# Kernel optimization log

Hardware: AMD Instinct MI355X
Metric: run time of the kernel (lower is better)

The kernel has to match this reference:

```python
import jax, jax.numpy as jnp
import numpy as np

N_HEAD = 16
N_FEAT = 1024
D_K = N_FEAT // N_HEAD  # 64
BLOCK_SIZE = 32
MAX_BLOCKS = 512
CHUNK = 1024
OFFSET = 3072  # cache_seqlens[0]: frames already committed to the cache
SCALE = 0.02


def setup_inputs() -> dict:
    key = jax.random.key(0)
    ks = jax.random.split(key, 12)
    # logical -> physical block mapping: a fixed permutation (irregular access)
    rng = np.random.default_rng(0)
    block_table = jnp.asarray(rng.permutation(MAX_BLOCKS).astype(np.int32))[None, :]
    return {
        "x": jax.random.normal(ks[0], (1, CHUNK, N_FEAT), jnp.float32),
        "Wq": jax.random.normal(ks[1], (N_FEAT, N_FEAT), jnp.float32) * SCALE,
        "bq": jax.random.normal(ks[2], (N_FEAT,), jnp.float32) * SCALE,
        "Wk": jax.random.normal(ks[3], (N_FEAT, N_FEAT), jnp.float32) * SCALE,
        "bk": jax.random.normal(ks[4], (N_FEAT,), jnp.float32) * SCALE,
        "Wv": jax.random.normal(ks[5], (N_FEAT, N_FEAT), jnp.float32) * SCALE,
        "bv": jax.random.normal(ks[6], (N_FEAT,), jnp.float32) * SCALE,
        "Wo": jax.random.normal(ks[7], (N_FEAT, N_FEAT), jnp.float32) * SCALE,
        "bo": jax.random.normal(ks[8], (N_FEAT,), jnp.float32) * SCALE,
        "k_cache": jax.random.normal(ks[9], (MAX_BLOCKS, BLOCK_SIZE, N_HEAD, D_K), jnp.float32),
        "v_cache": jax.random.normal(ks[10], (MAX_BLOCKS, BLOCK_SIZE, N_HEAD, D_K), jnp.float32),
        "block_table": block_table,
        "seqlen_offset": OFFSET,
    }


def reference(x, Wq, bq, Wk, bk, Wv, bv, Wo, bo, k_cache, v_cache, block_table, seqlen_offset):
    B, T, _ = x.shape  # B == 1 (streaming decode)
    # forward_qkv: Q/K/V projections, split into heads
    q = (x @ Wq + bq).reshape(B, T, N_HEAD, D_K).transpose(0, 2, 1, 3)  # (1,h,T,d)
    k_new = (x @ Wk + bk).reshape(B, T, N_HEAD, D_K)                    # (1,T,h,d)
    v_new = (x @ Wv + bv).reshape(B, T, N_HEAD, D_K)

    # _paged_write_kv: scatter the chunk frames into the physical block pool
    pos = seqlen_offset + jnp.arange(T)              # absolute frame indices
    phys = block_table[0, pos // BLOCK_SIZE]         # physical block per frame
    off = pos % BLOCK_SIZE                           # offset within block
    k_cache = k_cache.at[phys, off].set(k_new[0])
    v_cache = v_cache.at[phys, off].set(v_new[0])

    # _paged_gather_kv: gather all total_frames (old + just-written) frames
    total = seqlen_offset + T
    nblk = (total + BLOCK_SIZE - 1) // BLOCK_SIZE
    bids = block_table[0, :nblk]
    kf = k_cache[bids].reshape(-1, N_HEAD, D_K)[:total]  # (total, h, d)
    vf = v_cache[bids].reshape(-1, N_HEAD, D_K)[:total]

    # SDPA over the gathered K/V (no mask; softmax in fp32 as in the source)
    scores = jnp.einsum('bhqd,khd->bhqk', q, kf) / np.float32(np.sqrt(D_K))
    attn = jax.nn.softmax(scores.astype(jnp.float32), axis=-1).astype(x.dtype)
    ctx = jnp.einsum('bhqk,khd->bhqd', attn, vf)         # (1,h,T,d)

    # forward_attention tail: merge heads + output projection
    out = ctx.transpose(0, 2, 1, 3).reshape(B, T, N_HEAD * D_K) @ Wo + bo
    return out
```

## Files before the change

### kernel.cpp

```cpp
#include <hip/hip_runtime.h>
#include <hip/hip_bf16.h>

#define NFEAT 1024
#define NHEAD 16
#define DK 64
#define TCHUNK 1024
#define MAXTOK 4096
#define NSPLIT 4

using bf16x8 = __attribute__((ext_vector_type(8))) short;
using f32x4  = __attribute__((ext_vector_type(4))) float;

__device__ __forceinline__ short f2bf(float f) {
    __hip_bfloat16 h = __float2bfloat16(f);
    return *reinterpret_cast<short*>(&h);
}

__device__ __forceinline__ float exp2fast(float x) {
    return __builtin_amdgcn_exp2f(x);
}

#define QSCALE 0.1803368801f

__global__ __launch_bounds__(256) void pack_kernel(
    const float* __restrict__ x,
    const float* __restrict__ Wq, const float* __restrict__ Wk,
    const float* __restrict__ Wv, const float* __restrict__ Wo,
    const float* __restrict__ kc, const float* __restrict__ vc,
    const int* __restrict__ btab, const int* __restrict__ soff,
    short* __restrict__ xb, short* __restrict__ Wt,
    short* __restrict__ kg, short* __restrict__ vt) {
    const int b = blockIdx.x;
    const int t = threadIdx.x;
    if (b < 1024) {
        __shared__ short T[64][72];
        const int w = b >> 8, tile = b & 255;
        const int k0 = (tile >> 4) << 6, n0 = (tile & 15) << 6;
        const float* W = (w == 0) ? Wq : (w == 1) ? Wk : (w == 2) ? Wv : Wo;
        const int r = t >> 2, cs = (t & 3) << 4;
        #pragma unroll
        for (int u = 0; u < 4; ++u) {
            float4 v = *reinterpret_cast<const float4*>(
                &W[(size_t)(k0 + r) * NFEAT + n0 + cs + u * 4]);
            T[cs + u * 4 + 0][r] = f2bf(v.x);
            T[cs + u * 4 + 1][r] = f2bf(v.y);
            T[cs + u * 4 + 2][r] = f2bf(v.z);
            T[cs + u * 4 + 3][r] = f2bf(v.w);
        }
        __syncthreads();
        const int c = t >> 2, rs = (t & 3) << 4;
        bf16x8 a0 = *reinterpret_cast<const bf16x8*>(&T[c][rs]);
        bf16x8 a1 = *reinterpret_cast<const bf16x8*>(&T[c][rs + 8]);
        size_t drow = (size_t)(w * 1024 + n0 + c) * NFEAT + k0 + rs;
        *reinterpret_cast<bf16x8*>(&Wt[drow]) = a0;
        *reinterpret_cast<bf16x8*>(&Wt[drow + 8]) = a1;
    } else if (b < 1152) {
        const int e0 = ((b - 1024) * 256 + t) * 32;
        #pragma unroll
        for (int u = 0; u < 4; ++u) {
            float4 v0 = *reinterpret_cast<const float4*>(&x[e0 + u * 8]);
            float4 v1 = *reinterpret_cast<const float4*>(&x[e0 + u * 8 + 4]);
            bf16x8 o;
            o[0] = f2bf(v0.x); o[1] = f2bf(v0.y); o[2] = f2bf(v0.z); o[3] = f2bf(v0.w);
            o[4] = f2bf(v1.x); o[5] = f2bf(v1.y); o[6] = f2bf(v1.z); o[7] = f2bf(v1.w);
            *reinterpret_cast<bf16x8*>(&xb[e0 + u * 8]) = o;
        }
    } else {
        __shared__ short TV[64][72];
        const int cb = b - 1152;
        const int h = cb & 15;
        const int t0 = (cb >> 4) << 6;
        const int offset = soff[0];
        const int row = t >> 2, ds = (t & 3) << 4;
        const int tok = t0 + row;
        short kv[16], vv[16];
        if (tok < offset) {
            int phys = btab[tok >> 5];
            size_t base = ((size_t)(phys * 32 + (tok & 31)) * NHEAD + h) * DK + ds;
            #pragma unroll
            for (int u = 0; u < 4; ++u) {
                float4 kf = *reinterpret_cast<const float4*>(&kc[base + u * 4]);
                float4 vf = *reinterpret_cast<const float4*>(&vc[base + u * 4]);
                kv[u * 4 + 0] = f2bf(kf.x); kv[u * 4 + 1] = f2bf(kf.y);
                kv[u * 4 + 2] = f2bf(kf.z); kv[u * 4 + 3] = f2bf(kf.w);
                vv[u * 4 + 0] = f2bf(vf.x); vv[u * 4 + 1] = f2bf(vf.y);
                vv[u * 4 + 2] = f2bf(vf.z); vv[u * 4 + 3] = f2bf(vf.w);
            }
        } else {
            #pragma unroll
            for (int e = 0; e < 16; ++e) { kv[e] = 0; vv[e] = 0; }
        }
        {
            bf16x8 a, bb;
            #pragma unroll
            for (int e = 0; e < 8; ++e) { a[e] = kv[e]; bb[e] = kv[8 + e]; }
            size_t kb = ((size_t)h * MAXTOK + tok) * DK + ds;
            *reinterpret_cast<bf16x8*>(&kg[kb]) = a;
            *reinterpret_cast<bf16x8*>(&kg[kb + 8]) = bb;
        }
        #pragma unroll
        for (int e = 0; e < 16; ++e) TV[ds + e][row] = vv[e];
        __syncthreads();
        {
            const int d = t >> 2, ts = (t & 3) << 4;
            bf16x8 a = *reinterpret_cast<const bf16x8*>(&TV[d][ts]);
            bf16x8 bb = *reinterpret_cast<const bf16x8*>(&TV[d][ts + 8]);
            size_t vb = ((size_t)h * DK + d) * MAXTOK + t0 + ts;
            *reinterpret_cast<bf16x8*>(&vt[vb]) = a;
            *reinterpret_cast<bf16x8*>(&vt[vb + 8]) = bb;
        }
    }
}

__global__ __launch_bounds__(256) void qkv_gemm(
    const short* __restrict__ xb, const short* __restrict__ Wt,
    const float* __restrict__ bq, const float* __restrict__ bk,
    const float* __restrict__ bv, const int* __restrict__ soff,
    short* __restrict__ qbuf, short* __restrict__ kg, short* __restrict__ vt) {
    __shared__ short As[64][72];
    __shared__ short Bs[128][72];
    const int tid = threadIdx.x;
    const int lane = tid & 63;
    const int w = tid >> 6;
    const int l15 = lane & 15, lg = lane >> 4;
    const int wr = w >> 1, wc = w & 1;
    const int m0 = blockIdx.y << 6, n0 = blockIdx.x << 7;
    const int sel = n0 >> 10;
    const float* bias = (sel == 0) ? bq : (sel == 1) ? bk : bv;

    f32x4 acc[2][4];
    #pragma unroll
    for (int i = 0; i < 2; ++i)
        #pragma unroll
        for (int j = 0; j < 4; ++j) acc[i][j] = (f32x4){0.f, 0.f, 0.f, 0.f};

    for (int k0 = 0; k0 < NFEAT; k0 += 64) {
        #pragma unroll
        for (int r = 0; r < 2; ++r) {
            int f = tid + (r << 8);
            int row = f >> 3, kc = (f & 7) << 3;
            *reinterpret_cast<bf16x8*>(&As[row][kc]) =
                *reinterpret_cast<const bf16x8*>(&xb[(size_t)(m0 + row) * NFEAT + k0 + kc]);
        }
        #pragma unroll
        for (int r = 0; r < 4; ++r) {
            int f = tid + (r << 8);
            int row = f >> 3, kc = (f & 7) << 3;
            *reinterpret_cast<bf16x8*>(&Bs[row][kc]) =
                *reinterpret_cast<const bf16x8*>(&Wt[(size_t)(n0 + row) * NFEAT + k0 + kc]);
        }
        __syncthreads();
        #pragma unroll
        for (int kk = 0; kk < 2; ++kk) {
            bf16x8 am[2], bn[4];
            #pragma unroll
            for (int mi = 0; mi < 2; ++mi)
                am[mi] = *reinterpret_cast<const bf16x8*>(
                    &As[wr * 32 + mi * 16 + l15][kk * 32 + lg * 8]);
            #pragma unroll
            for (int ni = 0; ni < 4; ++ni)
                bn[ni] = *reinterpret_cast<const bf16x8*>(
                    &Bs[wc * 64 + ni * 16 + l15][kk * 32 + lg * 8]);
            #pragma unroll
            for (int mi = 0; mi < 2; ++mi)
                #pragma unroll
                for (int ni = 0; ni < 4; ++ni)
                    acc[mi][ni] = __builtin_amdgcn_mfma_f32_16x16x32_bf16(
                        am[mi], bn[ni], acc[mi][ni], 0, 0, 0);
        }
        __syncthreads();
    }
    const int offs = soff[0];
    #pragma unroll
    for (int mi = 0; mi < 2; ++mi)
        #pragma unroll
        for (int rr = 0; rr < 4; ++rr) {
            int m = m0 + wr * 32 + mi * 16 + lg * 4 + rr;
            #pragma unroll
            for (int ni = 0; ni < 4; ++ni) {
                int n = n0 + wc * 64 + ni * 16 + l15;
                float v = acc[mi][ni][rr] + bias[n & 1023];
                if (sel == 0) {
                    qbuf[(size_t)m * NFEAT + n] = f2bf(v * QSCALE);
                } else if (sel == 1) {
                    int nn = n - 1024, hh = nn >> 6, dd = nn & 63;
                    kg[((size_t)hh * MAXTOK + offs + m) * DK + dd] = f2bf(v);
                } else {
                    int nn = n - 2048, hh = nn >> 6, dd = nn & 63;
                    vt[((size_t)hh * DK + dd) * MAXTOK + offs + m] = f2bf(v);
                }
            }
        }
}

__global__ __launch_bounds__(256) void out_gemm(
    const short* __restrict__ ctxb, const short* __restrict__ Wt,
    const float* __restrict__ bo, float* __restrict__ out) {
    __shared__ short As[64][72];
    __shared__ short Bs[64][72];
    const int tid = threadIdx.x;
    const int lane = tid & 63;
    const int w = tid >> 6;
    const int l15 = lane & 15, lg = lane >> 4;
    const int wr = w >> 1, wc = w & 1;
    const int m0 = blockIdx.y << 6, n0 = blockIdx.x << 6;

    f32x4 acc[2][2];
    #pragma unroll
    for (int i = 0; i < 2; ++i)
        #pragma unroll
        for (int j = 0; j < 2; ++j) acc[i][j] = (f32x4){0.f, 0.f, 0.f, 0.f};

    for (int k0 = 0; k0 < NFEAT; k0 += 64) {
        #pragma unroll
        for (int r = 0; r < 2; ++r) {
            int f = tid + (r << 8);
            int row = f >> 3, kc = (f & 7) << 3;
            *reinterpret_cast<bf16x8*>(&As[row][kc]) =
                *reinterpret_cast<const bf16x8*>(&ctxb[(size_t)(m0 + row) * NFEAT + k0 + kc]);
            *reinterpret_cast<bf16x8*>(&Bs[row][kc]) =
                *reinterpret_cast<const bf16x8*>(
                    &Wt[(size_t)(3072 + n0 + row) * NFEAT + k0 + kc]);
        }
        __syncthreads();
        #pragma unroll
        for (int kk = 0; kk < 2; ++kk) {
            bf16x8 am[2], bn[2];
            #pragma unroll
            for (int mi = 0; mi < 2; ++mi)
                am[mi] = *reinterpret_cast<const bf16x8*>(
                    &As[wr * 32 + mi * 16 + l15][kk * 32 + lg * 8]);
            #pragma unroll
            for (int ni = 0; ni < 2; ++ni)
                bn[ni] = *reinterpret_cast<const bf16x8*>(
                    &Bs[wc * 32 + ni * 16 + l15][kk * 32 + lg * 8]);
            #pragma unroll
            for (int mi = 0; mi < 2; ++mi)
                #pragma unroll
                for (int ni = 0; ni < 2; ++ni)
                    acc[mi][ni] = __builtin_amdgcn_mfma_f32_16x16x32_bf16(
                        am[mi], bn[ni], acc[mi][ni], 0, 0, 0);
        }
        __syncthreads();
    }
    #pragma unroll
    for (int mi = 0; mi < 2; ++mi)
        #pragma unroll
        for (int rr = 0; rr < 4; ++rr) {
            int m = m0 + wr * 32 + mi * 16 + lg * 4 + rr;
            #pragma unroll
            for (int ni = 0; ni < 2; ++ni) {
                int n = n0 + wc * 32 + ni * 16 + l15;
                out[(size_t)m * NFEAT + n] = acc[mi][ni][rr] + bo[n];
            }
        }
}

__global__ __launch_bounds__(128, 2) void attn_mfma(
    const short* __restrict__ qbuf, const short* __restrict__ kg,
    const short* __restrict__ vt, const int* __restrict__ soff,
    float* __restrict__ pacc) {
    __shared__ short Ks[64][72];
    __shared__ short Vs[64][72];
    __shared__ short Ps[2][32][72];

    const int tid = threadIdx.x;
    const int lane = tid & 63;
    const int w = tid >> 6;
    const int l15 = lane & 15;
    const int lg = lane >> 4;
    const int h = blockIdx.x;
    const int qt = blockIdx.y;
    const int z = blockIdx.z;
    const int offset = soff[0];
    const int total = offset + TCHUNK;
    const int ntiles = (total + 63) >> 6;
    const int NT = (ntiles + NSPLIT - 1) / NSPLIT;
    const int tbase = z * NT;
    const int tend = min(tbase + NT, ntiles);

    const int srow = tid >> 1;
    const int sseg = (tid & 1) << 5;

    const short* kbase = kg + (size_t)h * MAXTOK * DK;
    const short* vbase = vt + (size_t)h * DK * MAXTOK;

    bf16x8 aq[2][2];
    #pragma unroll
    for (int set = 0; set < 2; ++set) {
        size_t qrow = (size_t)(qt * 64 + w * 32 + set * 16 + l15) * NFEAT + h * DK;
        aq[set][0] = *reinterpret_cast<const bf16x8*>(&qbuf[qrow + lg * 8]);
        aq[set][1] = *reinterpret_cast<const bf16x8*>(&qbuf[qrow + 32 + lg * 8]);
    }

    bf16x8 ones;
    #pragma unroll
    for (int e = 0; e < 8; ++e) ones[e] = (short)0x3F80;

    float m[2][4];
    f32x4 acc[2][4], acc1[2];
    #pragma unroll
    for (int set = 0; set < 2; ++set) {
        #pragma unroll
        for (int r = 0; r < 4; ++r) m[set][r] = -1e30f;
        #pragma unroll
        for (int fc = 0; fc < 4; ++fc) acc[set][fc] = (f32x4){0.f, 0.f, 0.f, 0.f};
        acc1[set] = (f32x4){0.f, 0.f, 0.f, 0.f};
    }

    bf16x8 kr[4], vr[4];
    if (tbase < tend) {
        int tok0 = tbase << 6;
        #pragma unroll
        for (int j = 0; j < 4; ++j) {
            kr[j] = *reinterpret_cast<const bf16x8*>(
                &kbase[(size_t)(tok0 + srow) * DK + sseg + j * 8]);
            vr[j] = *reinterpret_cast<const bf16x8*>(
                &vbase[(size_t)srow * MAXTOK + tok0 + sseg + j * 8]);
        }
    }

    for (int t = tbase; t < tend; ++t) {
        __syncthreads();
        #pragma unroll
        for (int j = 0; j < 4; ++j) {
            *reinterpret_cast<bf16x8*>(&Ks[srow][sseg + j * 8]) = kr[j];
            *reinterpret_cast<bf16x8*>(&Vs[srow][sseg + j * 8]) = vr[j];
        }
        __syncthreads();
        if (t + 1 < tend) {
            int tok0 = (t + 1) << 6;
            #pragma unroll
            for (int j = 0; j < 4; ++j) {
                kr[j] = *reinterpret_cast<const bf16x8*>(
                    &kbase[(size_t)(tok0 + srow) * DK + sseg + j * 8]);
                vr[j] = *reinterpret_cast<const bf16x8*>(
                    &vbase[(size_t)srow * MAXTOK + tok0 + sseg + j * 8]);
            }
        }

        const int kt0 = t << 6;
        bf16x8 kb0[4], kb1[4];
        #pragma unroll
        for (int fc = 0; fc < 4; ++fc) {
            kb0[fc] = *reinterpret_cast<const bf16x8*>(&Ks[fc * 16 + l15][lg * 8]);
            kb1[fc] = *reinterpret_cast<const bf16x8*>(&Ks[fc * 16 + l15][32 + lg * 8]);
        }
        #pragma unroll
        for (int set = 0; set < 2; ++set) {
            f32x4 s[4];
            __builtin_amdgcn_s_setprio(1);
            #pragma unroll
            for (int fc = 0; fc < 4; ++fc) {
                s[fc] = __builtin_amdgcn_mfma_f32_16x16x32_bf16(
                    aq[set][0], kb0[fc], (f32x4){0.f, 0.f, 0.f, 0.f}, 0, 0, 0);
                s[fc] = __builtin_amdgcn_mfma_f32_16x16x32_bf16(
                    aq[set][1], kb1[fc], s[fc], 0, 0, 0);
            }
            __builtin_amdgcn_s_setprio(0);
            if (kt0 + 64 > total) {
                #pragma unroll
                for (int fc = 0; fc < 4; ++fc) {
                    bool valid = (kt0 + fc * 16 + l15) < total;
                    #pragma unroll
                    for (int r = 0; r < 4; ++r)
                        s[fc][r] = valid ? s[fc][r] : -1e30f;
                }
            }
            float lm[4];
            #pragma unroll
            for (int r = 0; r < 4; ++r)
                lm[r] = fmaxf(fmaxf(s[0][r], s[1][r]), fmaxf(s[2][r], s[3][r]));
            bool ok = lm[0] <= m[set][0] + 8.f && lm[1] <= m[set][1] + 8.f &&
                      lm[2] <= m[set][2] + 8.f && lm[3] <= m[set][3] + 8.f;
            if (!__all(ok)) {
                #pragma unroll
                for (int r = 0; r < 4; ++r) {
                    float tm = lm[r];
                    tm = fmaxf(tm, __shfl_xor(tm, 1));
                    tm = fmaxf(tm, __shfl_xor(tm, 2));
                    tm = fmaxf(tm, __shfl_xor(tm, 4));
                    tm = fmaxf(tm, __shfl_xor(tm, 8));
                    float mn = fmaxf(m[set][r], tm);
                    float sc = exp2fast(m[set][r] - mn);
                    m[set][r] = mn;
                    acc1[set][r] *= sc;
                    #pragma unroll
                    for (int fc = 0; fc < 4; ++fc) acc[set][fc][r] *= sc;
                }
            }
            #pragma unroll
            for (int fc = 0; fc < 4; ++fc)
                #pragma unroll
                for (int r = 0; r < 4; ++r)
                    Ps[w][set * 16 + lg * 4 + r][l15 + 16 * fc] =
                        f2bf(exp2fast(s[fc][r] - m[set][r]));
        }
        #pragma unroll
        for (int ks = 0; ks < 2; ++ks) {
            bf16x8 pa0 = *reinterpret_cast<const bf16x8*>(
                &Ps[w][l15][ks * 32 + lg * 8]);
            bf16x8 pa1 = *reinterpret_cast<const bf16x8*>(
                &Ps[w][16 + l15][ks * 32 + lg * 8]);
            __builtin_amdgcn_s_setprio(1);
            acc1[0] = __builtin_amdgcn_mfma_f32_16x16x32_bf16(pa0, ones, acc1[0], 0, 0, 0);
            acc1[1] = __builtin_amdgcn_mfma_f32_16x16x32_bf16(pa1, ones, acc1[1], 0, 0, 0);
            #pragma unroll
            for (int fc = 0; fc < 4; ++fc) {
                bf16x8 bv = *reinterpret_cast<const bf16x8*>(
                    &Vs[fc * 16 + l15][ks * 32 + lg * 8]);
                acc[0][fc] = __builtin_amdgcn_mfma_f32_16x16x32_bf16(pa0, bv, acc[0][fc], 0, 0, 0);
                acc[1][fc] = __builtin_amdgcn_mfma_f32_16x16x32_bf16(pa1, bv, acc[1][fc], 0, 0, 0);
            }
            __builtin_amdgcn_s_setprio(0);
        }
    }

    const size_t pbase = (((size_t)z * NHEAD + h) * 16 + qt) * 4224;
    #pragma unroll
    for (int set = 0; set < 2; ++set)
        #pragma unroll
        for (int r = 0; r < 4; ++r) {
            int q = w * 32 + set * 16 + lg * 4 + r;
            if (l15 == 0) {
                pacc[pbase + 4096 + q] = m[set][r];
                pacc[pbase + 4160 + q] = acc1[set][r];
            }
            #pragma unroll
            for (int fc = 0; fc < 4; ++fc)
                pacc[pbase + q * 64 + l15 + 16 * fc] = acc[set][fc][r];
        }
}

__global__ __launch_bounds__(256) void merge_ctx(
    const float* __restrict__ pacc, short* __restrict__ ctxb) {
    const int h = blockIdx.x, qt = blockIdx.y;
    const int t = threadIdx.x;
    const int q = t >> 2, ds = (t & 3) << 4;
    size_t b[NSPLIT];
    float mz[NSPLIT], lz[NSPLIT];
    float M = -1e30f;
    #pragma unroll
    for (int z = 0; z < NSPLIT; ++z) {
        b[z] = (((size_t)z * NHEAD + h) * 16 + qt) * 4224;
        mz[z] = pacc[b[z] + 4096 + q];
        lz[z] = pacc[b[z] + 4160 + q];
        M = fmaxf(M, mz[z]);
    }
    float L = 0.f, ez[NSPLIT];
    #pragma unroll
    for (int z = 0; z < NSPLIT; ++z) {
        ez[z] = __builtin_amdgcn_exp2f(mz[z] - M);
        L += lz[z] * ez[z];
    }
    float inv = 1.f / L;
    bf16x8 o0, o1;
    #pragma unroll
    for (int j = 0; j < 8; ++j) {
        float v = 0.f;
        #pragma unroll
        for (int z = 0; z < NSPLIT; ++z)
            v += pacc[b[z] + q * 64 + ds + j] * ez[z];
        o0[j] = f2bf(v * inv);
    }
    #pragma unroll
    for (int j = 0; j < 8; ++j) {
        float v = 0.f;
        #pragma unroll
        for (int z = 0; z < NSPLIT; ++z)
            v += pacc[b[z] + q * 64 + ds + 8 + j] * ez[z];
        o1[j] = f2bf(v * inv);
    }
    size_t ob = (size_t)(qt * 64 + q) * NFEAT + h * DK + ds;
    *reinterpret_cast<bf16x8*>(&ctxb[ob]) = o0;
    *reinterpret_cast<bf16x8*>(&ctxb[ob + 8]) = o1;
}

extern "C" void kernel_launch(void* const* d_in, const int* in_sizes, int n_in,
                              void* d_out, int out_size, void* d_ws, size_t ws_size,
                              hipStream_t stream) {
    const float* x   = (const float*)d_in[0];
    const float* Wq  = (const float*)d_in[1];
    const float* bq  = (const float*)d_in[2];
    const float* Wk  = (const float*)d_in[3];
    const float* bk  = (const float*)d_in[4];
    const float* Wv  = (const float*)d_in[5];
    const float* bv  = (const float*)d_in[6];
    const float* Wo  = (const float*)d_in[7];
    const float* bo  = (const float*)d_in[8];
    const float* kc  = (const float*)d_in[9];
    const float* vc  = (const float*)d_in[10];
    const int*   bt  = (const int*)d_in[11];
    const int*   so  = (const int*)d_in[12];

    short* xb   = (short*)d_ws;
    short* Wt   = xb + (size_t)1024 * 1024;
    short* qbuf = Wt + (size_t)4096 * 1024;
    short* kg   = qbuf + (size_t)1024 * 1024;
    short* vtb  = kg + (size_t)NHEAD * MAXTOK * DK;
    float* pacc = (float*)(vtb + (size_t)NHEAD * DK * MAXTOK);
    short* ctxb = (short*)(pacc + (size_t)NSPLIT * 256 * 4224);

    pack_kernel<<<dim3(1920), 256, 0, stream>>>(x, Wq, Wk, Wv, Wo, kc, vc, bt, so,
                                                xb, Wt, kg, vtb);
    qkv_gemm<<<dim3(24, 16), 256, 0, stream>>>(xb, Wt, bq, bk, bv, so,
                                               qbuf, kg, vtb);
    attn_mfma<<<dim3(16, 16, NSPLIT), 128, 0, stream>>>(qbuf, kg, vtb, so, pacc);
    merge_ctx<<<dim3(16, 16), 256, 0, stream>>>(pacc, ctxb);
    out_gemm<<<dim3(16, 16), 256, 0, stream>>>(ctxb, Wt, bo, (float*)d_out);
}
```

Measured before the change: 104.7 us.

## Rework attention inner loop with 32x32 MFMA and register-resident probabilities

The attention kernel moves from 16x16x32 MFMA tiles to 32x32x16 tiles and computes S transposed (K times Q), so each lane owns one query column. Probabilities are packed to bf16 in registers and exchanged across half-waves with shuffles rather than round-tripped through shared memory. The row sum is now accumulated in scalar registers instead of an extra MFMA against a ones vector. The intent is to cut LDS traffic, the P staging buffer and the MFMA issue count. In exchange the code relies on precise 32x32 output lane layouts, adds shuffles to the rescale path, and raises register pressure from the 16-wide accumulators.

```diff
diff --git a/kernel.cpp b/kernel.cpp
--- a/kernel.cpp
+++ b/kernel.cpp
@@ -10,6 +10,8 @@
 
 using bf16x8 = __attribute__((ext_vector_type(8))) short;
 using f32x4  = __attribute__((ext_vector_type(4))) float;
+using f32x16 = __attribute__((ext_vector_type(16))) float;
+using u32x4  = __attribute__((ext_vector_type(4))) unsigned int;
 
 __device__ __forceinline__ short f2bf(float f) {
     __hip_bfloat16 h = __float2bfloat16(f);
@@ -18,6 +20,12 @@
 
 __device__ __forceinline__ float exp2fast(float x) {
     return __builtin_amdgcn_exp2f(x);
+}
+
+__device__ __forceinline__ unsigned int pack2bf(float a, float b) {
+    unsigned int lo = (unsigned int)(unsigned short)f2bf(a);
+    unsigned int hi = (unsigned int)(unsigned short)f2bf(b);
+    return lo | (hi << 16);
 }
 
 #define QSCALE 0.1803368801f
@@ -262,13 +270,12 @@
     float* __restrict__ pacc) {
     __shared__ short Ks[64][72];
     __shared__ short Vs[64][72];
-    __shared__ short Ps[2][32][72];
 
     const int tid = threadIdx.x;
     const int lane = tid & 63;
     const int w = tid >> 6;
-    const int l15 = lane & 15;
-    const int lg = lane >> 4;
+    const int l31 = lane & 31;
+    const int hi = lane >> 5;
     const int h = blockIdx.x;
     const int qt = blockIdx.y;
     const int z = blockIdx.z;
@@ -285,28 +292,18 @@
     const short* kbase = kg + (size_t)h * MAXTOK * DK;
     const short* vbase = vt + (size_t)h * DK * MAXTOK;
 
-    bf16x8 aq[2][2];
-    #pragma unroll
-    for (int set = 0; set < 2; ++set) {
-        size_t qrow = (size_t)(qt * 64 + w * 32 + set * 16 + l15) * NFEAT + h * DK;
-        aq[set][0] = *reinterpret_cast<const bf16x8*>(&qbuf[qrow + lg * 8]);
-        aq[set][1] = *reinterpret_cast<const bf16x8*>(&qbuf[qrow + 32 + lg * 8]);
-    }
-
-    bf16x8 ones;
-    #pragma unroll
-    for (int e = 0; e < 8; ++e) ones[e] = (short)0x3F80;
-
-    float m[2][4];
-    f32x4 acc[2][4], acc1[2];
-    #pragma unroll
-    for (int set = 0; set < 2; ++set) {
-        #pragma unroll
-        for (int r = 0; r < 4; ++r) m[set][r] = -1e30f;
-        #pragma unroll
-        for (int fc = 0; fc < 4; ++fc) acc[set][fc] = (f32x4){0.f, 0.f, 0.f, 0.f};
-        acc1[set] = (f32x4){0.f, 0.f, 0.f, 0.f};
-    }
+    bf16x8 qf[4];
+    {
+        size_t qrow = (size_t)(qt * 64 + w * 32 + l31) * NFEAT + h * DK;
+        #pragma unroll
+        for (int j = 0; j < 4; ++j)
+            qf[j] = *reinterpret_cast<const bf16x8*>(&qbuf[qrow + j * 16 + hi * 8]);
+    }
+
+    float m = -1e30f, lsum = 0.f;
+    f32x16 accA, accB;
+    #pragma unroll
+    for (int i = 0; i < 16; ++i) { accA[i] = 0.f; accB[i] = 0.f; }
 
     bf16x8 kr[4], vr[4];
     if (tbase < tend) {
@@ -340,96 +337,93 @@
         }
 
         const int kt0 = t << 6;
-        bf16x8 kb0[4], kb1[4];
-        #pragma unroll
-        for (int fc = 0; fc < 4; ++fc) {
-            kb0[fc] = *reinterpret_cast<const bf16x8*>(&Ks[fc * 16 + l15][lg * 8]);
-            kb1[fc] = *reinterpret_cast<const bf16x8*>(&Ks[fc * 16 + l15][32 + lg * 8]);
-        }
-        #pragma unroll
-        for (int set = 0; set < 2; ++set) {
-            f32x4 s[4];
+        f32x16 st0, st1;
+        #pragma unroll
+        for (int i = 0; i < 16; ++i) { st0[i] = 0.f; st1[i] = 0.f; }
+        __builtin_amdgcn_s_setprio(1);
+        #pragma unroll
+        for (int j = 0; j < 4; ++j) {
+            bf16x8 ka0 = *reinterpret_cast<const bf16x8*>(&Ks[l31][j * 16 + hi * 8]);
+            bf16x8 ka1 = *reinterpret_cast<const bf16x8*>(&Ks[32 + l31][j * 16 + hi * 8]);
+            st0 = __builtin_amdgcn_mfma_f32_32x32x16_bf16(ka0, qf[j], st0, 0, 0, 0);
+            st1 = __builtin_amdgcn_mfma_f32_32x32x16_bf16(ka1, qf[j], st1, 0, 0, 0);
+        }
+        __builtin_amdgcn_s_setprio(0);
+        if (kt0 + 64 > total) {
+            #pragma unroll
+            for (int r = 0; r < 16; ++r) {
+                int crow = (r & 3) + 8 * (r >> 2) + 4 * hi;
+                if (kt0 + crow >= total) st0[r] = -1e30f;
+                if (kt0 + 32 + crow >= total) st1[r] = -1e30f;
+            }
+        }
+        float lm = st0[0];
+        #pragma unroll
+        for (int r = 1; r < 16; ++r) lm = fmaxf(lm, st0[r]);
+        #pragma unroll
+        for (int r = 0; r < 16; ++r) lm = fmaxf(lm, st1[r]);
+        float full = fmaxf(lm, __shfl_xor(lm, 32));
+        if (!__all(full <= m + 8.f)) {
+            float mn = fmaxf(m, full);
+            float sc = exp2fast(m - mn);
+            m = mn;
+            lsum *= sc;
+            #pragma unroll
+            for (int r = 0; r < 16; ++r) {
+                int crow = (r & 3) + 8 * (r >> 2) + 4 * hi;
+                float scr = __shfl(sc, crow);
+                accA[r] *= scr;
+                accB[r] *= scr;
+            }
+        }
+        unsigned int pk0[8], pk1[8];
+        #pragma unroll
+        for (int c = 0; c < 8; ++c) {
+            float a0 = exp2fast(st0[2 * c] - m);
+            float a1 = exp2fast(st0[2 * c + 1] - m);
+            float b0 = exp2fast(st1[2 * c] - m);
+            float b1 = exp2fast(st1[2 * c + 1] - m);
+            lsum += (a0 + a1) + (b0 + b1);
+            pk0[c] = pack2bf(a0, a1);
+            pk1[c] = pack2bf(b0, b1);
+        }
+        #pragma unroll
+        for (int ks = 0; ks < 4; ++ks) {
+            const int b4 = (ks & 1) * 4;
+            unsigned int w0, w1, w2, w3;
+            if (ks < 2) { w0 = pk0[b4]; w1 = pk0[b4 + 1]; w2 = pk0[b4 + 2]; w3 = pk0[b4 + 3]; }
+            else        { w0 = pk1[b4]; w1 = pk1[b4 + 1]; w2 = pk1[b4 + 2]; w3 = pk1[b4 + 3]; }
+            unsigned int x0 = __shfl_xor(hi ? w0 : w2, 32);
+            unsigned int x1 = __shfl_xor(hi ? w1 : w3, 32);
+            u32x4 uu;
+            uu[0] = hi ? x0 : w0;
+            uu[1] = hi ? x1 : w1;
+            uu[2] = hi ? w2 : x0;
+            uu[3] = hi ? w3 : x1;
+            bf16x8 pa = __builtin_bit_cast(bf16x8, uu);
+            bf16x8 bv0 = *reinterpret_cast<const bf16x8*>(&Vs[l31][ks * 16 + hi * 8]);
+            bf16x8 bv1 = *reinterpret_cast<const bf16x8*>(&Vs[32 + l31][ks * 16 + hi * 8]);
             __builtin_amdgcn_s_setprio(1);
-            #pragma unroll
-            for (int fc = 0; fc < 4; ++fc) {
-                s[fc] = __builtin_amdgcn_mfma_f32_16x16x32_bf16(
-                    aq[set][0], kb0[fc], (f32x4){0.f, 0.f, 0.f, 0.f}, 0, 0, 0);
-                s[fc] = __builtin_amdgcn_mfma_f32_16x16x32_bf16(
-                    aq[set][1], kb1[fc], s[fc], 0, 0, 0);
-            }
+            accA = __builtin_amdgcn_mfma_f32_32x32x16_bf16(pa, bv0, accA, 0, 0, 0);
+            accB = __builtin_amdgcn_mfma_f32_32x32x16_bf16(pa, bv1, accB, 0, 0, 0);
             __builtin_amdgcn_s_setprio(0);
-            if (kt0 + 64 > total) {
-                #pragma unroll
-                for (int fc = 0; fc < 4; ++fc) {
-                    bool valid = (kt0 + fc * 16 + l15) < total;
-                    #pragma unroll
-                    for (int r = 0; r < 4; ++r)
-                        s[fc][r] = valid ? s[fc][r] : -1e30f;
-                }
-            }
-            float lm[4];
-            #pragma unroll
-            for (int r = 0; r < 4; ++r)
-                lm[r] = fmaxf(fmaxf(s[0][r], s[1][r]), fmaxf(s[2][r], s[3][r]));
-            bool ok = lm[0] <= m[set][0] + 8.f && lm[1] <= m[set][1] + 8.f &&
-                      lm[2] <= m[set][2] + 8.f && lm[3] <= m[set][3] + 8.f;
-            if (!__all(ok)) {
-                #pragma unroll
-                for (int r = 0; r < 4; ++r) {
-                    float tm = lm[r];
-                    tm = fmaxf(tm, __shfl_xor(tm, 1));
-                    tm = fmaxf(tm, __shfl_xor(tm, 2));
-                    tm = fmaxf(tm, __shfl_xor(tm, 4));
-                    tm = fmaxf(tm, __shfl_xor(tm, 8));
-                    float mn = fmaxf(m[set][r], tm);
-                    float sc = exp2fast(m[set][r] - mn);
-                    m[set][r] = mn;
-                    acc1[set][r] *= sc;
-                    #pragma unroll
-                    for (int fc = 0; fc < 4; ++fc) acc[set][fc][r] *= sc;
-                }
-            }
-            #pragma unroll
-            for (int fc = 0; fc < 4; ++fc)
-                #pragma unroll
-                for (int r = 0; r < 4; ++r)
-                    Ps[w][set * 16 + lg * 4 + r][l15 + 16 * fc] =
-                        f2bf(exp2fast(s[fc][r] - m[set][r]));
-        }
-        #pragma unroll
-        for (int ks = 0; ks < 2; ++ks) {
-            bf16x8 pa0 = *reinterpret_cast<const bf16x8*>(
-                &Ps[w][l15][ks * 32 + lg * 8]);
-            bf16x8 pa1 = *reinterpret_cast<const bf16x8*>(
-                &Ps[w][16 + l15][ks * 32 + lg * 8]);
-            __builtin_amdgcn_s_setprio(1);
-            acc1[0] = __builtin_amdgcn_mfma_f32_16x16x32_bf16(pa0, ones, acc1[0], 0, 0, 0);
-            acc1[1] = __builtin_amdgcn_mfma_f32_16x16x32_bf16(pa1, ones, acc1[1], 0, 0, 0);
-            #pragma unroll
-            for (int fc = 0; fc < 4; ++fc) {
-                bf16x8 bv = *reinterpret_cast<const bf16x8*>(
-                    &Vs[fc * 16 + l15][ks * 32 + lg * 8]);
-                acc[0][fc] = __builtin_amdgcn_mfma_f32_16x16x32_bf16(pa0, bv, acc[0][fc], 0, 0, 0);
-                acc[1][fc] = __builtin_amdgcn_mfma_f32_16x16x32_bf16(pa1, bv, acc[1][fc], 0, 0, 0);
-            }
-            __builtin_amdgcn_s_setprio(0);
-        }
-    }
-
+        }
+    }
+
+    float lt = lsum + __shfl_xor(lsum, 32);
     const size_t pbase = (((size_t)z * NHEAD + h) * 16 + qt) * 4224;
-    #pragma unroll
-    for (int set = 0; set < 2; ++set)
-        #pragma unroll
-        for (int r = 0; r < 4; ++r) {
-            int q = w * 32 + set * 16 + lg * 4 + r;
-            if (l15 == 0) {
-                pacc[pbase + 4096 + q] = m[set][r];
-                pacc[pbase + 4160 + q] = acc1[set][r];
-            }
-            #pragma unroll
-            for (int fc = 0; fc < 4; ++fc)
-                pacc[pbase + q * 64 + l15 + 16 * fc] = acc[set][fc][r];
-        }
+    if (hi == 0) {
+        int q = w * 32 + l31;
+        pacc[pbase + 4096 + q] = m;
+        pacc[pbase + 4160 + q] = lt;
+    }
+    #pragma unroll
+    for (int r = 0; r < 16; ++r) {
+        int crow = (r & 3) + 8 * (r >> 2) + 4 * hi;
+        int q = w * 32 + crow;
+        pacc[pbase + q * 64 + l31] = accA[r];
+        pacc[pbase + q * 64 + 32 + l31] = accB[r];
+    }
 }
 
 __global__ __launch_bounds__(256) void merge_ctx(
```

After: 100.6 us, median of 2. -3.9%, faster.
